# Kernel tuning notes

Measured on AMD Instinct MI355X. Metric: run time of the kernel, lower is better.

## Reference

```python
import jax, jax.numpy as jnp
import numpy as np

B, S, D, DEPTH = 2, 2048, 1024, 4
NUM_LEAVES = 2 ** DEPTH          # 16
NUM_DEC = NUM_LEAVES - 1         # 15


def setup_inputs() -> dict:
    key = jax.random.key(0)
    k1, k2, k3, k4, k5 = jax.random.split(key, 5)
    scale = 1.0 / np.sqrt(D)
    return {
        "x": jax.random.normal(k1, (B, S, D), dtype=jnp.float32),
        "dec_w": jax.random.normal(k2, (NUM_DEC, D), dtype=jnp.float32) * scale,
        "dec_b": jax.random.normal(k3, (NUM_DEC,), dtype=jnp.float32) * scale,
        "leaf_w": jax.random.normal(k4, (NUM_LEAVES, D, D), dtype=jnp.float32) * scale,  # [leaf, out, in] (torch Linear layout)
        "leaf_b": jax.random.normal(k5, (NUM_LEAVES, D), dtype=jnp.float32) * scale,
    }


def reference(x, dec_w, dec_b, leaf_w, leaf_b):
    num_leaves = leaf_w.shape[0]
    num_dec = num_leaves - 1
    # All decision-node sigmoids in one batched GEMM: [B,S,num_dec]
    dec = jax.nn.sigmoid(jnp.einsum("bsd,nd->bsn", x, dec_w) + dec_b)
    # Faithful to the original: each tree slot is multiplied exactly once by its
    # direct parent's decision (left child: p, right child: 1-p).
    leaf_idx = np.arange(num_dec, 2 * num_leaves - 1)      # slots holding leaf probs
    parent = (leaf_idx - 1) // 2                           # [num_leaves]
    is_left = (leaf_idx % 2 == 1)                          # [num_leaves]
    dec_p = dec[..., parent]                               # [B,S,num_leaves]
    leaf_probs = jnp.where(jnp.asarray(is_left), dec_p, 1.0 - dec_p)
    # All leaf MLPs as one batched GEMM: [B,S,L,D]
    leaf_out = jnp.einsum("bsd,lod->bslo", x, leaf_w) + leaf_b
    # Probability-weighted sum over leaves -> [B,S,D]
    return jnp.einsum("bslo,bsl->bso", leaf_out, leaf_probs)
```

## Files before the change

kernel.cpp:

```cpp
#include <hip/hip_runtime.h>
#include <stdint.h>


#define M_TOK 4096
#define DDIM  1024
#define KFLAT 9216

typedef __bf16 bf16x8 __attribute__((ext_vector_type(8)));
typedef float  f32x4  __attribute__((ext_vector_type(4)));
typedef unsigned short u16x4 __attribute__((ext_vector_type(4)));
typedef unsigned short u16x8 __attribute__((ext_vector_type(8)));

#define GLB(p) ((const __attribute__((address_space(1))) void*)(p))
#define LDS(p) ((__attribute__((address_space(3))) void*)(p))

__device__ __forceinline__ unsigned short f2bf(float f) {
    union { float f; uint32_t u; } v; v.f = f;
    uint32_t u = v.u;
    return (unsigned short)((u + 0x7fffu + ((u >> 16) & 1u)) >> 16);
}

__device__ __forceinline__ bf16x8 asbf(f32x4 v) {
    bf16x8 r; __builtin_memcpy(&r, &v, 16); return r;
}

template<int OFF>
__device__ __forceinline__ f32x4 dsr(uint32_t a) {
    f32x4 r;
    asm volatile("ds_read_b128 %0, %1 offset:%c2" : "=v"(r) : "v"(a), "i"(OFF));
    return r;
}

__global__ __launch_bounds__(256) void prep_dec_kernel(
    const float* __restrict__ x, const float* __restrict__ dec_w,
    const float* __restrict__ dec_b, const float* __restrict__ lw,
    const float* __restrict__ lb, unsigned short* __restrict__ wp,
    float* __restrict__ bw, unsigned short* __restrict__ xs,
    float* __restrict__ pmat)
{
    if (blockIdx.x < 1024) {
        int idx = blockIdx.x * 256 + threadIdx.x;
        int o  = idx >> 8;
        int k4 = (idx & 255) << 2;
        size_t src = (size_t)o * DDIM + k4;
        size_t dstb = (size_t)o * KFLAT + k4;
        float4 acc = make_float4(0.f, 0.f, 0.f, 0.f);
#pragma unroll
        for (int j = 0; j < 8; ++j) {
            const float4 a = *(const float4*)(lw + (size_t)(2*j)   * DDIM*DDIM + src);
            const float4 b = *(const float4*)(lw + (size_t)(2*j+1) * DDIM*DDIM + src);
            u16x4 d;
            d[0] = f2bf(a.x - b.x); d[1] = f2bf(a.y - b.y);
            d[2] = f2bf(a.z - b.z); d[3] = f2bf(a.w - b.w);
            *(u16x4*)(wp + dstb + (size_t)j * DDIM) = d;
            acc.x += b.x; acc.y += b.y; acc.z += b.z; acc.w += b.w;
        }
        u16x4 s;
        s[0] = f2bf(acc.x); s[1] = f2bf(acc.y); s[2] = f2bf(acc.z); s[3] = f2bf(acc.w);
        *(u16x4*)(wp + dstb + (size_t)8 * DDIM) = s;
        if ((idx & 255) == 0) {
            float sb = 0.f;
#pragma unroll
            for (int j = 0; j < 8; ++j) {
                float ba = lb[(2*j) * DDIM + o];
                float bb = lb[(2*j+1) * DDIM + o];
                bw[j * DDIM + o] = ba - bb;
                sb += bb;
            }
            bw[8 * DDIM + o] = sb;
        }
    } else {
        int m    = (blockIdx.x - 1024) * 4 + (threadIdx.x >> 6);
        int lane = threadIdx.x & 63;
        const float* xr = x + (size_t)m * DDIM + lane * 16;
        float xv[16];
        *(float4*)&xv[0]  = *(const float4*)(xr + 0);
        *(float4*)&xv[4]  = *(const float4*)(xr + 4);
        *(float4*)&xv[8]  = *(const float4*)(xr + 8);
        *(float4*)&xv[12] = *(const float4*)(xr + 12);
        float s[8];
#pragma unroll
        for (int j = 0; j < 8; ++j) {
            const float* wr = dec_w + (size_t)(7 + j) * DDIM + lane * 16;
            float a = 0.f;
#pragma unroll
            for (int i = 0; i < 16; i += 4) {
                float4 wv = *(const float4*)(wr + i);
                a = fmaf(xv[i], wv.x, fmaf(xv[i+1], wv.y, fmaf(xv[i+2], wv.z, fmaf(xv[i+3], wv.w, a))));
            }
            s[j] = a;
        }
#pragma unroll
        for (int j = 0; j < 8; ++j)
#pragma unroll
            for (int off = 32; off > 0; off >>= 1)
                s[j] += __shfl_xor(s[j], off);
        float p[8];
#pragma unroll
        for (int j = 0; j < 8; ++j)
            p[j] = 1.0f / (1.0f + expf(-(s[j] + dec_b[7 + j])));
        if (lane == 0) {
#pragma unroll
            for (int j = 0; j < 8; ++j)
                pmat[(size_t)m * 8 + j] = p[j];
        }
#pragma unroll
        for (int j = 0; j < 9; ++j) {
            float pj = (j < 8) ? p[j] : 1.0f;
            unsigned short* dst = xs + (size_t)m * KFLAT + j * DDIM + lane * 16;
#pragma unroll
            for (int c = 0; c < 2; ++c) {
                u16x8 o;
#pragma unroll
                for (int e = 0; e < 8; ++e) o[e] = f2bf(pj * xv[c * 8 + e]);
                *(u16x8*)(dst + c * 8) = o;
            }
        }
    }
}


#define WAITV4 asm volatile("s_waitcnt vmcnt(4)" ::: "memory")
#define WAITV0 asm volatile("s_waitcnt vmcnt(0)" ::: "memory")
#define BARR   __builtin_amdgcn_s_barrier()
#define LGKM0  do { asm volatile("s_waitcnt lgkmcnt(0)" ::: "memory"); \
                    __builtin_amdgcn_sched_barrier(0); } while(0)

#define READ_AV(q, b) do { \
    av[0][0] = dsr<(b)*32768 + (2*(q)+0)*2048>(baseA0); \
    av[0][1] = dsr<(b)*32768 + (2*(q)+0)*2048>(baseA1); \
    av[1][0] = dsr<(b)*32768 + (2*(q)+1)*2048>(baseA0); \
    av[1][1] = dsr<(b)*32768 + (2*(q)+1)*2048>(baseA1); \
} while(0)

#define READ_BV(b) do { \
    bv[0][0] = dsr<(b)*32768 + 0*2048>(baseB0); bv[0][1] = dsr<(b)*32768 + 0*2048>(baseB1); \
    bv[1][0] = dsr<(b)*32768 + 1*2048>(baseB0); bv[1][1] = dsr<(b)*32768 + 1*2048>(baseB1); \
    bv[2][0] = dsr<(b)*32768 + 2*2048>(baseB0); bv[2][1] = dsr<(b)*32768 + 2*2048>(baseB1); \
    bv[3][0] = dsr<(b)*32768 + 3*2048>(baseB0); bv[3][1] = dsr<(b)*32768 + 3*2048>(baseB1); \
} while(0)

#define MFMA_Q(q) do { \
    __builtin_amdgcn_s_setprio(1); \
    _Pragma("unroll") \
    for (int mfl = 0; mfl < 2; ++mfl) { \
        _Pragma("unroll") \
        for (int j = 0; j < 4; ++j) { \
            acc[2*(q)+mfl][j] = __builtin_amdgcn_mfma_f32_16x16x32_bf16(asbf(av[mfl][0]), asbf(bv[j][0]), acc[2*(q)+mfl][j], 0, 0, 0); \
            acc[2*(q)+mfl][j] = __builtin_amdgcn_mfma_f32_16x16x32_bf16(asbf(av[mfl][1]), asbf(bv[j][1]), acc[2*(q)+mfl][j], 0, 0, 0); \
        } \
    } \
    __builtin_amdgcn_s_setprio(0); \
} while(0)

__global__ __launch_bounds__(512, 2) void tree_gemm4(
    const unsigned short* __restrict__ xs,
    const unsigned short* __restrict__ wp,
    float* __restrict__ out,
    float* __restrict__ parts,
    int KG)
{
    extern __shared__ char smem[];
    const int tid  = threadIdx.x;
    const int lane = tid & 63;
    const int w    = tid >> 6;
    const int wm   = w >> 2, wn = w & 3;
    const int ra   = lane & 15;
    const int g16  = lane >> 4;

    const int bx  = blockIdx.x;
    const int xcd = bx & 7, ii = bx >> 3;
    const int nt  = xcd >> 1;
    const int mt  = (xcd & 1) * 8 + ii;
    const int m0  = mt * 256, n0 = nt * 256;
    const int g   = blockIdx.y;
    const int k0  = g * KG;
    const int NI  = KG >> 7;

    uint32_t sbase = (uint32_t)(uintptr_t)(__attribute__((address_space(3))) char*)smem;

    const uint32_t colb0 = (uint32_t)((g16 ^ (ra & 7)) << 4);
    const uint32_t colb1 = colb0 ^ 64;
    const uint32_t baseA0 = sbase + wm * 16384 + ra * 128 + colb0;
    const uint32_t baseA1 = sbase + wm * 16384 + ra * 128 + colb1;
    const uint32_t baseB0 = sbase + 65536 + wn * 8192 + ra * 128 + colb0;
    const uint32_t baseB1 = sbase + 65536 + wn * 8192 + ra * 128 + colb1;

    const int kel = (((lane & 7) ^ (lane >> 3)) & 7) * 8;
    const int rA  = w * 8 + (lane >> 3);

    auto stageA = [&](int buf, int tt, int hh) {
        const unsigned short* s0 = xs + (size_t)(m0 + hh * 128 + rA) * KFLAT + (k0 + tt * 64 + kel);
        char* d0 = smem + buf * 32768 + hh * 16384 + w * 1024;
        __builtin_amdgcn_global_load_lds(GLB(s0), LDS(d0), 16, 0, 0);
        __builtin_amdgcn_global_load_lds(GLB(s0 + (size_t)64 * KFLAT), LDS(d0 + 8192), 16, 0, 0);
    };
    auto stageB = [&](int buf, int tt, int hh) {
        const unsigned short* s0 = wp + (size_t)(n0 + hh * 128 + rA) * KFLAT + (k0 + tt * 64 + kel);
        char* d0 = smem + 65536 + buf * 32768 + hh * 16384 + w * 1024;
        __builtin_amdgcn_global_load_lds(GLB(s0), LDS(d0), 16, 0, 0);
        __builtin_amdgcn_global_load_lds(GLB(s0 + (size_t)64 * KFLAT), LDS(d0 + 8192), 16, 0, 0);
    };

    f32x4 acc[8][4] = {};
    f32x4 av[2][2], bv[4][2];

    stageA(0, 0, 0); stageA(0, 0, 1);
    stageB(0, 0, 0); stageB(0, 0, 1);
    stageB(1, 1, 0); stageB(1, 1, 1);
    WAITV4;
    BARR;

    for (int i = 0; i < NI; ++i) {
        const int t = 2 * i;
        const bool on = (i + 1 < NI);

        READ_BV(0); READ_AV(0, 0);
        stageA(1, t + 1, 0); stageA(1, t + 1, 1);
        BARR; LGKM0; MFMA_Q(0); BARR;
        READ_AV(1, 0);
        if (on) stageB(0, t + 2, 0);
        BARR; LGKM0; MFMA_Q(1); BARR;
        READ_AV(2, 0);
        if (on) stageB(0, t + 2, 1);
        BARR; LGKM0; MFMA_Q(2); BARR;
        READ_AV(3, 0);
        BARR; LGKM0; MFMA_Q(3);
        if (on) { WAITV4; } else { WAITV0; }
        BARR;

        READ_BV(1); READ_AV(0, 1);
        if (on) { stageA(0, t + 2, 0); stageA(0, t + 2, 1); }
        BARR; LGKM0; MFMA_Q(0); BARR;
        READ_AV(1, 1);
        if (on) stageB(1, t + 3, 0);
        BARR; LGKM0; MFMA_Q(1); BARR;
        READ_AV(2, 1);
        if (on) stageB(1, t + 3, 1);
        BARR; LGKM0; MFMA_Q(2); BARR;
        READ_AV(3, 1);
        BARR; LGKM0; MFMA_Q(3);
        if (on) WAITV4;
        BARR;
    }

    float* dst = (g == 0) ? out : parts + (size_t)(g - 1) * M_TOK * DDIM;
#pragma unroll
    for (int mf = 0; mf < 8; ++mf)
#pragma unroll
        for (int e = 0; e < 4; ++e) {
            int row = m0 + wm * 128 + mf * 16 + g16 * 4 + e;
#pragma unroll
            for (int j = 0; j < 4; ++j)
                dst[(size_t)row * DDIM + n0 + wn * 64 + j * 16 + ra] = acc[mf][j][e];
        }
}

__global__ __launch_bounds__(256) void reduce2_kernel(
    float* __restrict__ out, const float* __restrict__ parts,
    const float* __restrict__ pmat, const float* __restrict__ bw, int np)
{
    size_t i = (size_t)blockIdx.x * 256 + threadIdx.x;
    int m   = (int)(i >> 8);
    int col = (int)(i & 255) * 4;
    float4 a = ((const float4*)out)[i];
    for (int p = 0; p < np; ++p) {
        float4 b = ((const float4*)(parts + (size_t)p * M_TOK * DDIM))[i];
        a.x += b.x; a.y += b.y; a.z += b.z; a.w += b.w;
    }
    float4 pa = *(const float4*)(pmat + (size_t)m * 8);
    float4 pb = *(const float4*)(pmat + (size_t)m * 8 + 4);
    float4 bias = *(const float4*)(bw + 8 * DDIM + col);
#pragma unroll
    for (int l = 0; l < 8; ++l) {
        float pl = (l < 4) ? ((const float*)&pa)[l] : ((const float*)&pb)[l - 4];
        float4 bl = *(const float4*)(bw + l * DDIM + col);
        bias.x = fmaf(pl, bl.x, bias.x); bias.y = fmaf(pl, bl.y, bias.y);
        bias.z = fmaf(pl, bl.z, bias.z); bias.w = fmaf(pl, bl.w, bias.w);
    }
    a.x += bias.x; a.y += bias.y; a.z += bias.z; a.w += bias.w;
    ((float4*)out)[i] = a;
}

__global__ __launch_bounds__(256, 4) void tree_gemm3(
    const unsigned short* __restrict__ xs, const unsigned short* __restrict__ wp,
    const float* __restrict__ bw, const float* __restrict__ pmat,
    float* __restrict__ out, float* __restrict__ parts, int KG)
{
    __shared__ __align__(16) unsigned short Asm[2][128 * 32];
    __shared__ __align__(16) unsigned short Bsm[2][128 * 32];
    const int tid  = threadIdx.x;
    const int lane = tid & 63;
    const int w    = tid >> 6;
    const int wm   = w >> 1, wn = w & 1;
    const int bx   = blockIdx.x;
    const int xcd  = bx & 7;
    const int ii   = bx >> 3;
    const int mt   = xcd * 4 + (ii >> 3);
    const int nt   = ii & 7;
    const int m0   = mt * 128, n0 = nt * 128;
    const int g    = blockIdx.y;
    const int k0   = g * KG;
    const int ra   = lane & 15;
    const int kb   = (lane >> 4) * 8;
    f32x4 acc[4][4] = {};
    auto stage = [&](int buf, int t) {
#pragma unroll
        for (int c = 0; c < 2; ++c) {
            int row = w * 32 + c * 16 + (lane >> 2);
            int ke  = k0 + t * 32 + (lane & 3) * 8;
            const unsigned short* ga = xs + (size_t)(m0 + row) * KFLAT + ke;
            __builtin_amdgcn_global_load_lds(GLB(ga), LDS(&Asm[buf][w * 1024 + c * 512]), 16, 0, 0);
            const unsigned short* gb = wp + (size_t)(n0 + row) * KFLAT + ke;
            __builtin_amdgcn_global_load_lds(GLB(gb), LDS(&Bsm[buf][w * 1024 + c * 512]), 16, 0, 0);
        }
    };
    const int TOT = KG >> 5;
    stage(0, 0);
    __syncthreads();
    int cur = 0;
    for (int t = 0; t < TOT; ++t) {
        if (t + 1 < TOT) stage(cur ^ 1, t + 1);
        bf16x8 av2[4], bv2[4];
#pragma unroll
        for (int i2 = 0; i2 < 4; ++i2)
            av2[i2] = *(const bf16x8*)&Asm[cur][(wm * 64 + i2 * 16 + ra) * 32 + kb];
#pragma unroll
        for (int j = 0; j < 4; ++j)
            bv2[j] = *(const bf16x8*)&Bsm[cur][(wn * 64 + j * 16 + ra) * 32 + kb];
#pragma unroll
        for (int i2 = 0; i2 < 4; ++i2)
#pragma unroll
            for (int j = 0; j < 4; ++j)
                acc[i2][j] = __builtin_amdgcn_mfma_f32_16x16x32_bf16(av2[i2], bv2[j], acc[i2][j], 0, 0, 0);
        __syncthreads();
        cur ^= 1;
    }
    float* bsm = (float*)&Asm[0][0];
    if (g == 0) {
        for (int idx = tid; idx < 9 * 128; idx += 256)
            bsm[idx] = bw[(idx >> 7) * DDIM + n0 + (idx & 127)];
    }
    __syncthreads();
    float* dst = (g == 0) ? out : parts + (size_t)(g - 1) * M_TOK * DDIM;
#pragma unroll
    for (int i2 = 0; i2 < 4; ++i2)
#pragma unroll
        for (int r = 0; r < 4; ++r) {
            int row = m0 + wm * 64 + i2 * 16 + (lane >> 4) * 4 + r;
            float4 pa, pb;
            if (g == 0) {
                pa = *(const float4*)(pmat + (size_t)row * 8);
                pb = *(const float4*)(pmat + (size_t)row * 8 + 4);
            }
#pragma unroll
            for (int j = 0; j < 4; ++j) {
                int cl = wn * 64 + j * 16 + ra;
                float v = acc[i2][j][r];
                if (g == 0) {
                    v += pa.x * bsm[0 * 128 + cl] + pa.y * bsm[1 * 128 + cl]
                       + pa.z * bsm[2 * 128 + cl] + pa.w * bsm[3 * 128 + cl]
                       + pb.x * bsm[4 * 128 + cl] + pb.y * bsm[5 * 128 + cl]
                       + pb.z * bsm[6 * 128 + cl] + pb.w * bsm[7 * 128 + cl]
                       + bsm[8 * 128 + cl];
                }
                dst[(size_t)row * DDIM + n0 + cl] = v;
            }
        }
}

__global__ __launch_bounds__(256) void reduce_kernel(
    float* __restrict__ out, const float* __restrict__ parts, int np)
{
    size_t i = (size_t)blockIdx.x * 256 + threadIdx.x;
    float4 a = ((const float4*)out)[i];
    for (int p = 0; p < np; ++p) {
        float4 b = ((const float4*)(parts + (size_t)p * M_TOK * DDIM))[i];
        a.x += b.x; a.y += b.y; a.z += b.z; a.w += b.w;
    }
    ((float4*)out)[i] = a;
}

extern "C" void kernel_launch(void* const* d_in, const int* in_sizes, int n_in,
                              void* d_out, int out_size, void* d_ws, size_t ws_size,
                              hipStream_t stream) {
    (void)in_sizes; (void)n_in; (void)out_size;
    const float* x     = (const float*)d_in[0];
    const float* dec_w = (const float*)d_in[1];
    const float* dec_b = (const float*)d_in[2];
    const float* lw    = (const float*)d_in[3];
    const float* lb    = (const float*)d_in[4];
    float* out = (float*)d_out;
    uint8_t* w8 = (uint8_t*)d_ws;

    unsigned short* xs   = (unsigned short*)(w8);
    unsigned short* wp   = (unsigned short*)(w8 + 75497472);
    float*          bw   = (float*)(w8 + 94371840);
    float*          pmat = (float*)(w8 + 94408704);
    float*          parts= (float*)(w8 + 94539776);
    const size_t NEED3 = 94539776 + 2ull * 16777216;
    const size_t NEED4 = 94539776 + 3ull * 16777216;

    int ks = (ws_size >= NEED4) ? 4 : (ws_size >= NEED3) ? 3 : 0;
    if (!ks) return;

    prep_dec_kernel<<<2048, 256, 0, stream>>>(x, dec_w, dec_b, lw, lb, wp, bw, xs, pmat);

    hipError_t e = hipFuncSetAttribute(
        reinterpret_cast<const void*>(tree_gemm4),
        hipFuncAttributeMaxDynamicSharedMemorySize, 131072);
    if (e == hipSuccess) {
        tree_gemm4<<<dim3(64, ks), 512, 131072, stream>>>(xs, wp, out, parts, KFLAT / ks);
        reduce2_kernel<<<4096, 256, 0, stream>>>(out, parts, pmat, bw, ks - 1);
    } else {
        tree_gemm3<<<dim3(256, ks), 256, 0, stream>>>(xs, wp, bw, pmat, out, parts, KFLAT / ks);
        reduce_kernel<<<4096, 256, 0, stream>>>(out, parts, ks - 1);
    }
}
```

Baseline: 127.4 us.

## Add triple-buffered B pipeline GEMM with one barrier per k-tile

Adds a new tree_gemm5 kernel that uses 160KB of LDS: A tiles are double-buffered and B tiles triple-buffered. Each 64-wide k-step now needs a single vmcnt wait and barrier instead of a barrier around every MFMA quarter. A-fragment reads alternate between two register sets with partial lgkmcnt waits, so LDS reads overlap the MFMAs. The host tries this kernel first and falls back to the old tree_gemm4 path if the larger shared-memory request fails. The cost is more LDS and registers per block, and correctness depends on hand-counted vmcnt values.

```diff
diff --git a/kernel.cpp b/kernel.cpp
--- a/kernel.cpp
+++ b/kernel.cpp
@@ -119,45 +119,46 @@
     }
 }
 
-
+#define WAITV8 asm volatile("s_waitcnt vmcnt(8)" ::: "memory")
 #define WAITV4 asm volatile("s_waitcnt vmcnt(4)" ::: "memory")
 #define WAITV0 asm volatile("s_waitcnt vmcnt(0)" ::: "memory")
 #define BARR   __builtin_amdgcn_s_barrier()
 #define LGKM0  do { asm volatile("s_waitcnt lgkmcnt(0)" ::: "memory"); \
                     __builtin_amdgcn_sched_barrier(0); } while(0)
-
-#define READ_AV(q, b) do { \
-    av[0][0] = dsr<(b)*32768 + (2*(q)+0)*2048>(baseA0); \
-    av[0][1] = dsr<(b)*32768 + (2*(q)+0)*2048>(baseA1); \
-    av[1][0] = dsr<(b)*32768 + (2*(q)+1)*2048>(baseA0); \
-    av[1][1] = dsr<(b)*32768 + (2*(q)+1)*2048>(baseA1); \
-} while(0)
-
-#define READ_BV(b) do { \
-    bv[0][0] = dsr<(b)*32768 + 0*2048>(baseB0); bv[0][1] = dsr<(b)*32768 + 0*2048>(baseB1); \
-    bv[1][0] = dsr<(b)*32768 + 1*2048>(baseB0); bv[1][1] = dsr<(b)*32768 + 1*2048>(baseB1); \
-    bv[2][0] = dsr<(b)*32768 + 2*2048>(baseB0); bv[2][1] = dsr<(b)*32768 + 2*2048>(baseB1); \
-    bv[3][0] = dsr<(b)*32768 + 3*2048>(baseB0); bv[3][1] = dsr<(b)*32768 + 3*2048>(baseB1); \
-} while(0)
-
-#define MFMA_Q(q) do { \
+#define LGKM4  do { asm volatile("s_waitcnt lgkmcnt(4)" ::: "memory"); \
+                    __builtin_amdgcn_sched_barrier(0); } while(0)
+
+#define MFMA_Q(q, SET) do { \
     __builtin_amdgcn_s_setprio(1); \
     _Pragma("unroll") \
     for (int mfl = 0; mfl < 2; ++mfl) { \
         _Pragma("unroll") \
         for (int j = 0; j < 4; ++j) { \
-            acc[2*(q)+mfl][j] = __builtin_amdgcn_mfma_f32_16x16x32_bf16(asbf(av[mfl][0]), asbf(bv[j][0]), acc[2*(q)+mfl][j], 0, 0, 0); \
-            acc[2*(q)+mfl][j] = __builtin_amdgcn_mfma_f32_16x16x32_bf16(asbf(av[mfl][1]), asbf(bv[j][1]), acc[2*(q)+mfl][j], 0, 0, 0); \
+            acc[2*(q)+mfl][j] = __builtin_amdgcn_mfma_f32_16x16x32_bf16(asbf(SET[mfl][0]), asbf(bv[j][0]), acc[2*(q)+mfl][j], 0, 0, 0); \
+            acc[2*(q)+mfl][j] = __builtin_amdgcn_mfma_f32_16x16x32_bf16(asbf(SET[mfl][1]), asbf(bv[j][1]), acc[2*(q)+mfl][j], 0, 0, 0); \
         } \
     } \
     __builtin_amdgcn_s_setprio(0); \
 } while(0)
 
-__global__ __launch_bounds__(512, 2) void tree_gemm4(
+#define READ_A(SET, q) do { \
+    SET[0][0] = dsr<(2*(q)+0)*2048>(bA0); \
+    SET[0][1] = dsr<(2*(q)+0)*2048>(bA1); \
+    SET[1][0] = dsr<(2*(q)+1)*2048>(bA0); \
+    SET[1][1] = dsr<(2*(q)+1)*2048>(bA1); \
+} while(0)
+
+#define READ_B() do { \
+    bv[0][0] = dsr<0*2048>(bB0); bv[0][1] = dsr<0*2048>(bB1); \
+    bv[1][0] = dsr<1*2048>(bB0); bv[1][1] = dsr<1*2048>(bB1); \
+    bv[2][0] = dsr<2*2048>(bB0); bv[2][1] = dsr<2*2048>(bB1); \
+    bv[3][0] = dsr<3*2048>(bB0); bv[3][1] = dsr<3*2048>(bB1); \
+} while(0)
+
+__global__ __launch_bounds__(512, 2) void tree_gemm5(
     const unsigned short* __restrict__ xs,
     const unsigned short* __restrict__ wp,
-    float* __restrict__ out,
-    float* __restrict__ parts,
+    float* __restrict__ out, float* __restrict__ parts,
     int KG)
 {
     extern __shared__ char smem[];
@@ -175,16 +176,15 @@
     const int m0  = mt * 256, n0 = nt * 256;
     const int g   = blockIdx.y;
     const int k0  = g * KG;
-    const int NI  = KG >> 7;
+    const int NT  = KG >> 6;
 
     uint32_t sbase = (uint32_t)(uintptr_t)(__attribute__((address_space(3))) char*)smem;
-
     const uint32_t colb0 = (uint32_t)((g16 ^ (ra & 7)) << 4);
     const uint32_t colb1 = colb0 ^ 64;
-    const uint32_t baseA0 = sbase + wm * 16384 + ra * 128 + colb0;
-    const uint32_t baseA1 = sbase + wm * 16384 + ra * 128 + colb1;
-    const uint32_t baseB0 = sbase + 65536 + wn * 8192 + ra * 128 + colb0;
-    const uint32_t baseB1 = sbase + 65536 + wn * 8192 + ra * 128 + colb1;
+    const uint32_t baseA0s = sbase + wm * 16384 + ra * 128 + colb0;
+    const uint32_t baseA1s = sbase + wm * 16384 + ra * 128 + colb1;
+    const uint32_t baseB0s = sbase + 65536 + wn * 8192 + ra * 128 + colb0;
+    const uint32_t baseB1s = sbase + 65536 + wn * 8192 + ra * 128 + colb1;
 
     const int kel = (((lane & 7) ^ (lane >> 3)) & 7) * 8;
     const int rA  = w * 8 + (lane >> 3);
@@ -203,47 +203,141 @@
     };
 
     f32x4 acc[8][4] = {};
-    f32x4 av[2][2], bv[4][2];
-
+    f32x4 avA[2][2], avB[2][2], bv[4][2];
+
+    stageA(0, 0, 0); stageA(0, 0, 1);
+    stageB(0, 0, 0); stageB(0, 0, 1);
+    stageA(1, 1, 0); stageA(1, 1, 1);
+    stageB(1, 1, 0); stageB(1, 1, 1);
+    WAITV8;
+    BARR;
+
+    int bt = 0, bt2 = 2;
+    for (int t = 0; t < NT; ++t) {
+        if (t) {
+            if (t == NT - 1) { WAITV0; } else { WAITV4; }
+            BARR;
+        }
+        if (t + 1 < NT) { stageA((t + 1) & 1, t + 1, 0); stageA((t + 1) & 1, t + 1, 1); }
+        if (t + 2 < NT) { stageB(bt2, t + 2, 0); stageB(bt2, t + 2, 1); }
+
+        const uint32_t aoff = (uint32_t)(t & 1) << 15;
+        const uint32_t boff = (uint32_t)bt << 15;
+        const uint32_t bA0 = baseA0s + aoff, bA1 = baseA1s + aoff;
+        const uint32_t bB0 = baseB0s + boff, bB1 = baseB1s + boff;
+
+        READ_B();
+        READ_A(avA, 0);
+        READ_A(avB, 1);
+        LGKM4;  MFMA_Q(0, avA);
+        READ_A(avA, 2);
+        LGKM4;  MFMA_Q(1, avB);
+        READ_A(avB, 3);
+        LGKM4;  MFMA_Q(2, avA);
+        LGKM0;  MFMA_Q(3, avB);
+
+        bt  = (bt  == 2) ? 0 : bt  + 1;
+        bt2 = (bt2 == 2) ? 0 : bt2 + 1;
+    }
+
+    float* dst = (g == 0) ? out : parts + (size_t)(g - 1) * M_TOK * DDIM;
+#pragma unroll
+    for (int mf = 0; mf < 8; ++mf)
+#pragma unroll
+        for (int e = 0; e < 4; ++e) {
+            int row = m0 + wm * 128 + mf * 16 + g16 * 4 + e;
+#pragma unroll
+            for (int j = 0; j < 4; ++j)
+                dst[(size_t)row * DDIM + n0 + wn * 64 + j * 16 + ra] = acc[mf][j][e];
+        }
+}
+
+#define READ_AV4(q, b) do { \
+    avA[0][0] = dsr<(b)*32768 + (2*(q)+0)*2048>(baseA0); \
+    avA[0][1] = dsr<(b)*32768 + (2*(q)+0)*2048>(baseA1); \
+    avA[1][0] = dsr<(b)*32768 + (2*(q)+1)*2048>(baseA0); \
+    avA[1][1] = dsr<(b)*32768 + (2*(q)+1)*2048>(baseA1); \
+} while(0)
+
+#define READ_BV4(b) do { \
+    bv[0][0] = dsr<(b)*32768 + 0*2048>(baseB0); bv[0][1] = dsr<(b)*32768 + 0*2048>(baseB1); \
+    bv[1][0] = dsr<(b)*32768 + 1*2048>(baseB0); bv[1][1] = dsr<(b)*32768 + 1*2048>(baseB1); \
+    bv[2][0] = dsr<(b)*32768 + 2*2048>(baseB0); bv[2][1] = dsr<(b)*32768 + 2*2048>(baseB1); \
+    bv[3][0] = dsr<(b)*32768 + 3*2048>(baseB0); bv[3][1] = dsr<(b)*32768 + 3*2048>(baseB1); \
+} while(0)
+
+__global__ __launch_bounds__(512, 2) void tree_gemm4(
+    const unsigned short* __restrict__ xs, const unsigned short* __restrict__ wp,
+    float* __restrict__ out, float* __restrict__ parts, int KG)
+{
+    extern __shared__ char smem[];
+    const int tid  = threadIdx.x;
+    const int lane = tid & 63;
+    const int w    = tid >> 6;
+    const int wm   = w >> 2, wn = w & 3;
+    const int ra   = lane & 15;
+    const int g16  = lane >> 4;
+    const int bx  = blockIdx.x;
+    const int xcd = bx & 7, ii = bx >> 3;
+    const int nt  = xcd >> 1;
+    const int mt  = (xcd & 1) * 8 + ii;
+    const int m0  = mt * 256, n0 = nt * 256;
+    const int g   = blockIdx.y;
+    const int k0  = g * KG;
+    const int NI  = KG >> 7;
+    uint32_t sbase = (uint32_t)(uintptr_t)(__attribute__((address_space(3))) char*)smem;
+    const uint32_t colb0 = (uint32_t)((g16 ^ (ra & 7)) << 4);
+    const uint32_t colb1 = colb0 ^ 64;
+    const uint32_t baseA0 = sbase + wm * 16384 + ra * 128 + colb0;
+    const uint32_t baseA1 = sbase + wm * 16384 + ra * 128 + colb1;
+    const uint32_t baseB0 = sbase + 65536 + wn * 8192 + ra * 128 + colb0;
+    const uint32_t baseB1 = sbase + 65536 + wn * 8192 + ra * 128 + colb1;
+    const int kel = (((lane & 7) ^ (lane >> 3)) & 7) * 8;
+    const int rA  = w * 8 + (lane >> 3);
+    auto stageA = [&](int buf, int tt, int hh) {
+        const unsigned short* s0 = xs + (size_t)(m0 + hh * 128 + rA) * KFLAT + (k0 + tt * 64 + kel);
+        char* d0 = smem + buf * 32768 + hh * 16384 + w * 1024;
+        __builtin_amdgcn_global_load_lds(GLB(s0), LDS(d0), 16, 0, 0);
+        __builtin_amdgcn_global_load_lds(GLB(s0 + (size_t)64 * KFLAT), LDS(d0 + 8192), 16, 0, 0);
+    };
+    auto stageB = [&](int buf, int tt, int hh) {
+        const unsigned short* s0 = wp + (size_t)(n0 + hh * 128 + rA) * KFLAT + (k0 + tt * 64 + kel);
+        char* d0 = smem + 65536 + buf * 32768 + hh * 16384 + w * 1024;
+        __builtin_amdgcn_global_load_lds(GLB(s0), LDS(d0), 16, 0, 0);
+        __builtin_amdgcn_global_load_lds(GLB(s0 + (size_t)64 * KFLAT), LDS(d0 + 8192), 16, 0, 0);
+    };
+    f32x4 acc[8][4] = {};
+    f32x4 avA[2][2], bv[4][2];
     stageA(0, 0, 0); stageA(0, 0, 1);
     stageB(0, 0, 0); stageB(0, 0, 1);
     stageB(1, 1, 0); stageB(1, 1, 1);
-    WAITV4;
-    BARR;
-
+    WAITV4; BARR;
     for (int i = 0; i < NI; ++i) {
         const int t = 2 * i;
         const bool on = (i + 1 < NI);
-
-        READ_BV(0); READ_AV(0, 0);
+        READ_BV4(0); READ_AV4(0, 0);
         stageA(1, t + 1, 0); stageA(1, t + 1, 1);
-        BARR; LGKM0; MFMA_Q(0); BARR;
-        READ_AV(1, 0);
-        if (on) stageB(0, t + 2, 0);
-        BARR; LGKM0; MFMA_Q(1); BARR;
-        READ_AV(2, 0);
-        if (on) stageB(0, t + 2, 1);
-        BARR; LGKM0; MFMA_Q(2); BARR;
-        READ_AV(3, 0);
-        BARR; LGKM0; MFMA_Q(3);
+        BARR; LGKM0; MFMA_Q(0, avA); BARR;
+        READ_AV4(1, 0); if (on) stageB(0, t + 2, 0);
+        BARR; LGKM0; MFMA_Q(1, avA); BARR;
+        READ_AV4(2, 0); if (on) stageB(0, t + 2, 1);
+        BARR; LGKM0; MFMA_Q(2, avA); BARR;
+        READ_AV4(3, 0);
+        BARR; LGKM0; MFMA_Q(3, avA);
         if (on) { WAITV4; } else { WAITV0; }
         BARR;
-
-        READ_BV(1); READ_AV(0, 1);
+        READ_BV4(1); READ_AV4(0, 1);
         if (on) { stageA(0, t + 2, 0); stageA(0, t + 2, 1); }
-        BARR; LGKM0; MFMA_Q(0); BARR;
-        READ_AV(1, 1);
-        if (on) stageB(1, t + 3, 0);
-        BARR; LGKM0; MFMA_Q(1); BARR;
-        READ_AV(2, 1);
-        if (on) stageB(1, t + 3, 1);
-        BARR; LGKM0; MFMA_Q(2); BARR;
-        READ_AV(3, 1);
-        BARR; LGKM0; MFMA_Q(3);
+        BARR; LGKM0; MFMA_Q(0, avA); BARR;
+        READ_AV4(1, 1); if (on) stageB(1, t + 3, 0);
+        BARR; LGKM0; MFMA_Q(1, avA); BARR;
+        READ_AV4(2, 1); if (on) stageB(1, t + 3, 1);
+        BARR; LGKM0; MFMA_Q(2, avA); BARR;
+        READ_AV4(3, 1);
+        BARR; LGKM0; MFMA_Q(3, avA);
         if (on) WAITV4;
         BARR;
     }
-
     float* dst = (g == 0) ? out : parts + (size_t)(g - 1) * M_TOK * DDIM;
 #pragma unroll
     for (int mf = 0; mf < 8; ++mf)
@@ -406,10 +500,18 @@
 
     prep_dec_kernel<<<2048, 256, 0, stream>>>(x, dec_w, dec_b, lw, lb, wp, bw, xs, pmat);
 
-    hipError_t e = hipFuncSetAttribute(
+    hipError_t e5 = hipFuncSetAttribute(
+        reinterpret_cast<const void*>(tree_gemm5),
+        hipFuncAttributeMaxDynamicSharedMemorySize, 163840);
+    if (e5 == hipSuccess) {
+        tree_gemm5<<<dim3(64, ks), 512, 163840, stream>>>(xs, wp, out, parts, KFLAT / ks);
+        reduce2_kernel<<<4096, 256, 0, stream>>>(out, parts, pmat, bw, ks - 1);
+        return;
+    }
+    hipError_t e4 = hipFuncSetAttribute(
         reinterpret_cast<const void*>(tree_gemm4),
         hipFuncAttributeMaxDynamicSharedMemorySize, 131072);
-    if (e == hipSuccess) {
+    if (e4 == hipSuccess) {
         tree_gemm4<<<dim3(64, ks), 512, 131072, stream>>>(xs, wp, out, parts, KFLAT / ks);
         reduce2_kernel<<<4096, 256, 0, stream>>>(out, parts, pmat, bw, ks - 1);
     } else {
```

Measured after the change: 126.2 us. Within noise of the previous version (-0.9%).
